# Kernel optimization log

Hardware: AMD Instinct MI355X
Metric: run time of the kernel (lower is better)

The kernel has to match this reference:

```python
import jax, jax.numpy as jnp
import numpy as np

N_NODES = 100000
N_EDGES = 1600000
IN_SIZE = 256
HID = 64
HEADS = 2
OUT_SIZE = 16


def _gat_layer(x, W, a_l, a_r, b, src, dst, n_nodes, heads, feat):
    # x: [N, Din]; W: [Din, H*F]; a_l, a_r: [H, F]; b: [H*F]
    h = (x @ W).reshape(n_nodes, heads, feat)          # [N, H, F]
    el = jnp.sum(h * a_l, axis=-1)                     # [N, H]
    er = jnp.sum(h * a_r, axis=-1)                     # [N, H]
    e = jax.nn.leaky_relu(el[src] + er[dst], 0.2)      # [E, H]
    # segment softmax over incoming edges of each dst node
    m = jax.ops.segment_max(e, dst, num_segments=n_nodes)
    m = jnp.where(jnp.isfinite(m), m, 0.0)             # nodes with no in-edges
    p = jnp.exp(e - m[dst])                            # [E, H]
    s = jax.ops.segment_sum(p, dst, num_segments=n_nodes)
    alpha = p / (s[dst] + 1e-9)                        # [E, H]
    # scatter-add weighted source features
    out = jax.ops.segment_sum(alpha[:, :, None] * h[src], dst, num_segments=n_nodes)
    return out + b.reshape(1, heads, feat)             # [N, H, F]


def setup_inputs() -> dict:
    key = jax.random.key(0)
    ks = jax.random.split(key, 12)
    features = jax.random.normal(ks[0], (N_NODES, IN_SIZE), dtype=jnp.float32)
    src = jax.random.randint(ks[1], (N_EDGES,), 0, N_NODES, dtype=jnp.int32)
    dst = jax.random.randint(ks[2], (N_EDGES,), 0, N_NODES, dtype=jnp.int32)
    s1 = 1.0 / np.sqrt(IN_SIZE)
    s2 = 1.0 / np.sqrt(HID * HEADS)
    W1 = jax.random.normal(ks[3], (IN_SIZE, HEADS * HID), dtype=jnp.float32) * s1
    al1 = jax.random.normal(ks[4], (HEADS, HID), dtype=jnp.float32) * 0.1
    ar1 = jax.random.normal(ks[5], (HEADS, HID), dtype=jnp.float32) * 0.1
    b1 = jnp.zeros((HEADS * HID,), dtype=jnp.float32)
    W2 = jax.random.normal(ks[6], (HEADS * HID, HEADS * HID), dtype=jnp.float32) * s2
    al2 = jax.random.normal(ks[7], (HEADS, HID), dtype=jnp.float32) * 0.1
    ar2 = jax.random.normal(ks[8], (HEADS, HID), dtype=jnp.float32) * 0.1
    b2 = jnp.zeros((HEADS * HID,), dtype=jnp.float32)
    Wl = jax.random.normal(ks[9], (HEADS * HID, OUT_SIZE), dtype=jnp.float32) * s2
    bl = jnp.zeros((OUT_SIZE,), dtype=jnp.float32)
    return {"features": features, "src": src, "dst": dst,
            "W1": W1, "al1": al1, "ar1": ar1, "b1": b1,
            "W2": W2, "al2": al2, "ar2": ar2, "b2": b2,
            "Wl": Wl, "bl": bl}


def reference(features, src, dst, W1, al1, ar1, b1, W2, al2, ar2, b2, Wl, bl):
    n = features.shape[0]
    h = _gat_layer(features, W1, al1, ar1, b1.reshape(HEADS, HID).reshape(-1),
                   src, dst, n, HEADS, HID)
    h = jax.nn.elu(h.reshape(n, HEADS * HID))          # flatten(1) + ELU (dropout: eval)
    h = _gat_layer(h, W2, al2, ar2, b2, src, dst, n, HEADS, HID)
    h = jax.nn.elu(h.reshape(n, HEADS * HID))
    return h @ Wl + bl                                  # [N, OUT_SIZE]
```

## Files before the change

### kernel.cpp

```cpp
#include <hip/hip_runtime.h>
#include <hip/hip_fp16.h>

#define N_NODES 100000
#define N_EDGES 1600000
#define IN_SIZE 256
#define HID 64
#define HEADS 2
#define DMODEL 128
#define OUT_SZ 16

#define BSHIFT 9
#define BNODES 512
#define NB 196
#define CAP 16384
#define EPB 4096

typedef _Float16 f16x4 __attribute__((ext_vector_type(4)));
typedef _Float16 f16x8 __attribute__((ext_vector_type(8)));
typedef float f32x4 __attribute__((ext_vector_type(4)));


__global__ __launch_bounds__(256) void wt_fused_kernel(const float* __restrict__ W1,
                                                       _Float16* __restrict__ Wt1,
                                                       const float* __restrict__ W2,
                                                       _Float16* __restrict__ Wt2,
                                                       int* __restrict__ counts) {
    int tid = threadIdx.x;
    if (blockIdx.x == 0 && tid < NB) counts[tid] = 0;
    int i = blockIdx.x * 256 + tid;
    if (i < 128 * IN_SIZE) {
        int nr = i / IN_SIZE;
        int k = i - nr * IN_SIZE;
        Wt1[i] = (_Float16)W1[(size_t)k * 128 + nr];
    } else {
        int j = i - 128 * IN_SIZE;
        if (j < 128 * DMODEL) {
            int nr = j / DMODEL;
            int k = j - nr * DMODEL;
            Wt2[j] = (_Float16)W2[(size_t)k * 128 + nr];
        }
    }
}


__global__ __launch_bounds__(256) void bin_kernel(const int* __restrict__ src,
                                                  const int* __restrict__ dst,
                                                  int* __restrict__ counts,
                                                  int2* __restrict__ bucketbuf, int e) {
    __shared__ int hist[NB];
    __shared__ int base[NB];
    int tid = threadIdx.x;
    int start = blockIdx.x * EPB;
    for (int i = tid; i < NB; i += 256) hist[i] = 0;
    __syncthreads();
    int pack[16];
    #pragma unroll
    for (int i = 0; i < 16; i++) {
        int idx = start + i * 256 + tid;
        int p = -1;
        if (idx < e) {
            int b = dst[idx] >> BSHIFT;
            int r = atomicAdd(&hist[b], 1);
            p = (b << 16) | r;
        }
        pack[i] = p;
    }
    __syncthreads();
    for (int i = tid; i < NB; i += 256)
        base[i] = atomicAdd(&counts[i], hist[i]);
    __syncthreads();
    #pragma unroll
    for (int i = 0; i < 16; i++) {
        int idx = start + i * 256 + tid;
        int p = pack[i];
        if (p >= 0) {
            int b = p >> 16;
            int pos = base[b] + (p & 0xffff);
            if (pos < CAP)
                bucketbuf[(size_t)b * CAP + pos] = make_int2(src[idx], dst[idx]);
        }
    }
}


__global__ __launch_bounds__(256) void csr_kernel(const int2* __restrict__ bucketbuf,
                                                  const int* __restrict__ counts,
                                                  int* __restrict__ deg,
                                                  int* __restrict__ offs,
                                                  int* __restrict__ ssrc, int n) {
    __shared__ int hist[BNODES];
    __shared__ int cursor[BNODES];
    __shared__ int lds[256];
    int b = blockIdx.x;
    int tid = threadIdx.x;

    int t = (tid < NB) ? min(counts[tid], CAP) : 0;
    lds[tid] = t;
    __syncthreads();
    for (int off = 1; off < 256; off <<= 1) {
        int x = 0;
        if (tid >= off) x = lds[tid - off];
        __syncthreads();
        lds[tid] += x;
        __syncthreads();
    }
    int base = (b == 0) ? 0 : lds[b - 1];
    int cnt = min(counts[b], CAP);
    __syncthreads();

    int node0 = b << BSHIFT;
    const int2* ebuf = bucketbuf + (size_t)b * CAP;

    hist[tid] = 0;
    hist[tid + 256] = 0;
    __syncthreads();
    for (int i = tid; i < cnt; i += 256)
        atomicAdd(&hist[ebuf[i].y - node0], 1);
    __syncthreads();

    int h0 = hist[2 * tid], h1 = hist[2 * tid + 1];
    lds[tid] = h0 + h1;
    __syncthreads();
    for (int off = 1; off < 256; off <<= 1) {
        int x = 0;
        if (tid >= off) x = lds[tid - off];
        __syncthreads();
        lds[tid] += x;
        __syncthreads();
    }
    int excl = lds[tid] - (h0 + h1);
    cursor[2 * tid] = excl;
    cursor[2 * tid + 1] = excl + h0;
    int g0 = node0 + 2 * tid, g1 = g0 + 1;
    if (g0 < n) { deg[g0] = h0; offs[g0] = base + excl; }
    if (g1 < n) { deg[g1] = h1; offs[g1] = base + excl + h0; }
    __syncthreads();

    for (int i = tid; i < cnt; i += 256) {
        int2 ed = ebuf[i];
        int p = atomicAdd(&cursor[ed.y - node0], 1);
        ssrc[base + p] = ed.x;
    }
}


template <int K, bool F16IN>
__global__ __launch_bounds__(256) void gemm_attn_kernel(const void* __restrict__ Ap,
                                                        const _Float16* __restrict__ Wt,
                                                        const float* __restrict__ al,
                                                        const float* __restrict__ ar,
                                                        uint32_t* __restrict__ h16,
                                                        float* __restrict__ el,
                                                        float* __restrict__ er, int n) {
    __shared__ _Float16 As[64 * 72];
    __shared__ _Float16 Bs[128 * 72];
    int tid = threadIdx.x;
    int w = tid >> 6;
    int lane = tid & 63;
    int c = lane & 15;
    int quad = lane >> 4;
    int r0 = blockIdx.x * 64;

    f32x4 acc[8];
    #pragma unroll
    for (int t = 0; t < 8; t++) acc[t] = (f32x4){0.f, 0.f, 0.f, 0.f};

    for (int kt = 0; kt < K; kt += 64) {
        {
            int lr = tid >> 4;
            int lc = (tid & 15) * 4;
            #pragma unroll
            for (int q = 0; q < 4; q++) {
                int row = lr + 16 * q;
                int gr = r0 + row;
                if constexpr (F16IN) {
                    const uint32_t* Af = (const uint32_t*)Ap;
                    uint2 v = make_uint2(0u, 0u);
                    if (gr < n) v = *(const uint2*)(Af + (size_t)gr * (K / 2) + (kt + lc) / 2);
                    *(uint2*)(As + row * 72 + lc) = v;
                } else {
                    const float* Af = (const float*)Ap;
                    float4 v = make_float4(0.f, 0.f, 0.f, 0.f);
                    if (gr < n) v = *(const float4*)(Af + (size_t)gr * K + kt + lc);
                    f16x4 hv = {(_Float16)v.x, (_Float16)v.y, (_Float16)v.z, (_Float16)v.w};
                    *(f16x4*)(As + row * 72 + lc) = hv;
                }
            }
            int nr = tid >> 1;
            int kc = (tid & 1) * 32;
            const uint4* gsrc = (const uint4*)(Wt + (size_t)nr * K + kt + kc);
            uint4 v0 = gsrc[0];
            uint4 v1 = gsrc[1];
            uint4 v2 = gsrc[2];
            uint4 v3 = gsrc[3];
            *(uint4*)(Bs + nr * 72 + kc + 0)  = v0;
            *(uint4*)(Bs + nr * 72 + kc + 8)  = v1;
            *(uint4*)(Bs + nr * 72 + kc + 16) = v2;
            *(uint4*)(Bs + nr * 72 + kc + 24) = v3;
        }
        __syncthreads();

        #pragma unroll
        for (int kk = 0; kk < 64; kk += 32) {
            f16x8 a = *(const f16x8*)(As + (16 * w + c) * 72 + kk + quad * 8);
            #pragma unroll
            for (int t = 0; t < 8; t++) {
                f16x8 b = *(const f16x8*)(Bs + (16 * t + c) * 72 + kk + quad * 8);
                acc[t] = __builtin_amdgcn_mfma_f32_16x16x32_f16(a, b, acc[t], 0, 0, 0);
            }
        }
        __syncthreads();
    }

    #pragma unroll
    for (int i = 0; i < 4; i++) {
        int gr = r0 + 16 * w + quad * 4 + i;
        float el0 = 0.f, el1 = 0.f, er0 = 0.f, er1 = 0.f;
        #pragma unroll
        for (int t = 0; t < 8; t++) {
            float hv = acc[t][i];
            float alv = al[16 * t + c];
            float arv = ar[16 * t + c];
            if (t < 4) { el0 += hv * alv; er0 += hv * arv; }
            else       { el1 += hv * alv; er1 += hv * arv; }
        }
        #pragma unroll
        for (int off = 1; off < 16; off <<= 1) {
            el0 += __shfl_xor(el0, off);
            el1 += __shfl_xor(el1, off);
            er0 += __shfl_xor(er0, off);
            er1 += __shfl_xor(er1, off);
        }
        if (c == 0 && gr < n) {
            *(float2*)(el + 2 * gr) = make_float2(el0, el1);
            *(float2*)(er + 2 * gr) = make_float2(er0, er1);
        }
        #pragma unroll
        for (int t = 0; t < 8; t++) {
            float own = acc[t][i];
            float other = __shfl_xor(own, 1);
            if ((c & 1) == 0 && gr < n) {
                __half2 hh = __floats2half2_rn(own, other);
                h16[(size_t)gr * 64 + 8 * t + (c >> 1)] = *(const uint32_t*)&hh;
            }
        }
    }
}


__device__ __forceinline__ float edge_w(float2 e, float erh, int head) {
    float x = (head ? e.y : e.x) + erh;
    x = x >= 0.f ? x : 0.2f * x;
    return __expf(x);
}

__device__ __forceinline__ void acc8(uint4 u, float w, float* a) {
    union { uint4 u4; f16x8 h8; } cv;
    cv.u4 = u;
    #pragma unroll
    for (int i = 0; i < 8; i++)
        a[i] = fmaf((float)cv.h8[i], w, a[i]);
}

__global__ __launch_bounds__(256) void agg_kernel(const uint32_t* __restrict__ hb,
                                                  const int* __restrict__ ssrc,
                                                  const float* __restrict__ el,
                                                  const float* __restrict__ er,
                                                  const float* __restrict__ bias,
                                                  const int* __restrict__ offs,
                                                  const int* __restrict__ deg,
                                                  uint32_t* __restrict__ out16, int n) {
    int wid = (blockIdx.x * blockDim.x + threadIdx.x) >> 6;
    int lane = threadIdx.x & 63;
    if (wid >= n) return;
    int start = offs[wid];
    int d = deg[wid];
    int g = lane >> 4;
    int fl = lane & 15;
    int head = fl >> 3;

    float2 erv = *(const float2*)(er + 2 * wid);
    float erh = head ? erv.y : erv.x;

    const int* sp = ssrc + start;
    const float2* el2 = (const float2*)el;
    const char* hbb = (const char*)hb;
    uint32_t foff = (uint32_t)(fl << 4);

    float a[8];
    #pragma unroll
    for (int i = 0; i < 8; i++) a[i] = 0.f;
    float psum = 0.f;

    int j = 0;
    if (d >= 16) {
        int s0 = sp[g];
        int s1 = sp[4 + g];
        int s2 = sp[8 + g];
        int s3 = sp[12 + g];
        for (; j + 32 <= d; j += 16) {
            float2 e0 = el2[s0];
            uint4 u0 = *(const uint4*)(hbb + (((uint32_t)s0 << 8) + foff));
            float2 e1 = el2[s1];
            uint4 u1 = *(const uint4*)(hbb + (((uint32_t)s1 << 8) + foff));
            float2 e2 = el2[s2];
            uint4 u2 = *(const uint4*)(hbb + (((uint32_t)s2 << 8) + foff));
            float2 e3 = el2[s3];
            uint4 u3 = *(const uint4*)(hbb + (((uint32_t)s3 << 8) + foff));
            int ns0 = sp[j + 16 + g];
            int ns1 = sp[j + 20 + g];
            int ns2 = sp[j + 24 + g];
            int ns3 = sp[j + 28 + g];
            float w0 = edge_w(e0, erh, head);
            float w1 = edge_w(e1, erh, head);
            float w2 = edge_w(e2, erh, head);
            float w3 = edge_w(e3, erh, head);
            psum += (w0 + w1) + (w2 + w3);
            acc8(u0, w0, a);
            acc8(u1, w1, a);
            acc8(u2, w2, a);
            acc8(u3, w3, a);
            s0 = ns0; s1 = ns1; s2 = ns2; s3 = ns3;
        }
        {
            float2 e0 = el2[s0];
            uint4 u0 = *(const uint4*)(hbb + (((uint32_t)s0 << 8) + foff));
            float2 e1 = el2[s1];
            uint4 u1 = *(const uint4*)(hbb + (((uint32_t)s1 << 8) + foff));
            float2 e2 = el2[s2];
            uint4 u2 = *(const uint4*)(hbb + (((uint32_t)s2 << 8) + foff));
            float2 e3 = el2[s3];
            uint4 u3 = *(const uint4*)(hbb + (((uint32_t)s3 << 8) + foff));
            float w0 = edge_w(e0, erh, head);
            float w1 = edge_w(e1, erh, head);
            float w2 = edge_w(e2, erh, head);
            float w3 = edge_w(e3, erh, head);
            psum += (w0 + w1) + (w2 + w3);
            acc8(u0, w0, a);
            acc8(u1, w1, a);
            acc8(u2, w2, a);
            acc8(u3, w3, a);
            j += 16;
        }
    }
    if (j < d) {
        int last = d - 1;
        int i0 = j + g, i1 = j + 4 + g, i2 = j + 8 + g, i3 = j + 12 + g;
        int s0 = sp[min(i0, last)];
        int s1 = sp[min(i1, last)];
        int s2 = sp[min(i2, last)];
        int s3 = sp[min(i3, last)];
        float2 e0 = el2[s0];
        uint4 u0 = *(const uint4*)(hbb + (((uint32_t)s0 << 8) + foff));
        float2 e1 = el2[s1];
        uint4 u1 = *(const uint4*)(hbb + (((uint32_t)s1 << 8) + foff));
        float2 e2 = el2[s2];
        uint4 u2 = *(const uint4*)(hbb + (((uint32_t)s2 << 8) + foff));
        float2 e3 = el2[s3];
        uint4 u3 = *(const uint4*)(hbb + (((uint32_t)s3 << 8) + foff));
        float w0 = (i0 <= last) ? edge_w(e0, erh, head) : 0.f;
        float w1 = (i1 <= last) ? edge_w(e1, erh, head) : 0.f;
        float w2 = (i2 <= last) ? edge_w(e2, erh, head) : 0.f;
        float w3 = (i3 <= last) ? edge_w(e3, erh, head) : 0.f;
        psum += (w0 + w1) + (w2 + w3);
        acc8(u0, w0, a);
        acc8(u1, w1, a);
        acc8(u2, w2, a);
        acc8(u3, w3, a);
    }

    #pragma unroll
    for (int i = 0; i < 8; i++) {
        a[i] += __shfl_xor(a[i], 16);
        a[i] += __shfl_xor(a[i], 32);
    }
    psum += __shfl_xor(psum, 16);
    psum += __shfl_xor(psum, 32);

    if (lane < 16) {
        float inv = 1.f / (psum + 1e-9f);
        float4 b0 = *(const float4*)(bias + 8 * lane);
        float4 b1 = *(const float4*)(bias + 8 * lane + 4);
        float o[8];
        o[0] = fmaf(a[0], inv, b0.x);
        o[1] = fmaf(a[1], inv, b0.y);
        o[2] = fmaf(a[2], inv, b0.z);
        o[3] = fmaf(a[3], inv, b0.w);
        o[4] = fmaf(a[4], inv, b1.x);
        o[5] = fmaf(a[5], inv, b1.y);
        o[6] = fmaf(a[6], inv, b1.z);
        o[7] = fmaf(a[7], inv, b1.w);
        #pragma unroll
        for (int i = 0; i < 8; i++)
            o[i] = o[i] > 0.f ? o[i] : (__expf(o[i]) - 1.f);
        __half2 h01 = __floats2half2_rn(o[0], o[1]);
        __half2 h23 = __floats2half2_rn(o[2], o[3]);
        __half2 h45 = __floats2half2_rn(o[4], o[5]);
        __half2 h67 = __floats2half2_rn(o[6], o[7]);
        uint4 ov = make_uint4(*(const uint32_t*)&h01, *(const uint32_t*)&h23,
                              *(const uint32_t*)&h45, *(const uint32_t*)&h67);
        ((uint4*)(out16 + (size_t)wid * 64))[lane] = ov;
    }
}


__global__ __launch_bounds__(256) void final_kernel(const uint32_t* __restrict__ x16,
                                                    const float* __restrict__ Wl,
                                                    const float* __restrict__ bl,
                                                    float* __restrict__ out, int n) {
    __shared__ float Ws[DMODEL * OUT_SZ];
    __shared__ float bs[OUT_SZ];
    int tid = threadIdx.x;
    for (int i = tid; i < DMODEL * OUT_SZ / 4; i += 256)
        ((float4*)Ws)[i] = ((const float4*)Wl)[i];
    if (tid < OUT_SZ) bs[tid] = bl[tid];
    __syncthreads();
    int node = blockIdx.x * 16 + (tid >> 4);
    int c = tid & 15;
    if (node >= n) return;
    const uint2* xr = (const uint2*)(x16 + (size_t)node * 64);
    float acc = bs[c];
    #pragma unroll
    for (int kk = 0; kk < 32; kk++) {
        uint2 v = xr[kk];
        float2 f0 = __half22float2(*(const __half2*)&v.x);
        float2 f1 = __half22float2(*(const __half2*)&v.y);
        acc += f0.x * Ws[(4 * kk + 0) * OUT_SZ + c];
        acc += f0.y * Ws[(4 * kk + 1) * OUT_SZ + c];
        acc += f1.x * Ws[(4 * kk + 2) * OUT_SZ + c];
        acc += f1.y * Ws[(4 * kk + 3) * OUT_SZ + c];
    }
    out[(size_t)node * OUT_SZ + c] = acc;
}


extern "C" void kernel_launch(void* const* d_in, const int* in_sizes, int n_in,
                              void* d_out, int out_size, void* d_ws, size_t ws_size,
                              hipStream_t stream) {
    const float* features = (const float*)d_in[0];
    const int*   src      = (const int*)d_in[1];
    const int*   dst      = (const int*)d_in[2];
    const float* W1  = (const float*)d_in[3];
    const float* al1 = (const float*)d_in[4];
    const float* ar1 = (const float*)d_in[5];
    const float* b1  = (const float*)d_in[6];
    const float* W2  = (const float*)d_in[7];
    const float* al2 = (const float*)d_in[8];
    const float* ar2 = (const float*)d_in[9];
    const float* b2  = (const float*)d_in[10];
    const float* Wl  = (const float*)d_in[11];
    const float* bl  = (const float*)d_in[12];
    float* out = (float*)d_out;

    const int n = N_NODES, e = N_EDGES;

    char* w = (char*)d_ws;
    uint32_t* h16 = (uint32_t*)w;       w += (size_t)n * 64 * 4;
    uint32_t* x1  = (uint32_t*)w;       w += (size_t)n * 64 * 4;
    uint32_t* x2  = (uint32_t*)w;       w += 26 * 1024 * 1024;
    float* el   = (float*)w;            w += (size_t)n * 2 * 4;
    float* er   = (float*)w;            w += (size_t)n * 2 * 4;
    int* deg    = (int*)w;              w += 400128;
    int* offs   = (int*)w;              w += 400128;
    int* ssrc   = (int*)w;              w += (size_t)e * 4;
    int* counts = (int*)w;              w += 1024;
    _Float16* Wt1 = (_Float16*)w;       w += 128 * IN_SIZE * 2;
    _Float16* Wt2 = (_Float16*)w;       w += 128 * DMODEL * 2;
    int2* bucketbuf = (int2*)x2;

    const int binBlocks = (e + EPB - 1) / EPB;
    const int wtBlocks = (128 * IN_SIZE + 128 * DMODEL + 255) / 256;
    const int gemmBlocks = (n + 63) / 64;
    const int aggBlocks = (n + 3) / 4;
    const int finalBlocks = (n + 15) / 16;

    wt_fused_kernel<<<wtBlocks, 256, 0, stream>>>(W1, Wt1, W2, Wt2, counts);

    bin_kernel<<<binBlocks, 256, 0, stream>>>(src, dst, counts, bucketbuf, e);
    csr_kernel<<<NB, 256, 0, stream>>>(bucketbuf, counts, deg, offs, ssrc, n);

    gemm_attn_kernel<IN_SIZE, false><<<gemmBlocks, 256, 0, stream>>>(features, Wt1, al1, ar1,
                                                                     h16, el, er, n);
    agg_kernel<<<aggBlocks, 256, 0, stream>>>(h16, ssrc, el, er, b1, offs, deg, x1, n);

    gemm_attn_kernel<DMODEL, true><<<gemmBlocks, 256, 0, stream>>>(x1, Wt2, al2, ar2,
                                                                   h16, el, er, n);
    agg_kernel<<<aggBlocks, 256, 0, stream>>>(h16, ssrc, el, er, b2, offs, deg, x2, n);

    final_kernel<<<finalBlocks, 256, 0, stream>>>(x2, Wl, bl, out, n);

    (void)in_sizes; (void)n_in; (void)out_size; (void)ws_size;
}
```

Before: 421.5 us.

## Pack bucketed edges into 32-bit words and stage scatter through LDS

```diff
diff --git a/kernel.cpp b/kernel.cpp
--- a/kernel.cpp
+++ b/kernel.cpp
@@ -18,6 +18,7 @@
 typedef _Float16 f16x4 __attribute__((ext_vector_type(4)));
 typedef _Float16 f16x8 __attribute__((ext_vector_type(8)));
 typedef float f32x4 __attribute__((ext_vector_type(4)));
+
 
 
 __global__ __launch_bounds__(256) void wt_fused_kernel(const float* __restrict__ W1,
@@ -46,44 +47,67 @@
 __global__ __launch_bounds__(256) void bin_kernel(const int* __restrict__ src,
                                                   const int* __restrict__ dst,
                                                   int* __restrict__ counts,
-                                                  int2* __restrict__ bucketbuf, int e) {
+                                                  uint32_t* __restrict__ bucketbuf, int e) {
     __shared__ int hist[NB];
-    __shared__ int base[NB];
+    __shared__ int lbase[NB + 1];
+    __shared__ int gbase[NB];
+    __shared__ uint32_t sbuf[EPB];
+    __shared__ int lds[256];
     int tid = threadIdx.x;
     int start = blockIdx.x * EPB;
     for (int i = tid; i < NB; i += 256) hist[i] = 0;
     __syncthreads();
-    int pack[16];
+    int pr[16];
+    uint32_t pv[16];
     #pragma unroll
     for (int i = 0; i < 16; i++) {
         int idx = start + i * 256 + tid;
-        int p = -1;
+        pr[i] = -1;
         if (idx < e) {
-            int b = dst[idx] >> BSHIFT;
+            int d = dst[idx];
+            int s = src[idx];
+            int b = d >> BSHIFT;
             int r = atomicAdd(&hist[b], 1);
-            p = (b << 16) | r;
-        }
-        pack[i] = p;
-    }
-    __syncthreads();
-    for (int i = tid; i < NB; i += 256)
-        base[i] = atomicAdd(&counts[i], hist[i]);
+            pr[i] = (b << 16) | r;
+            pv[i] = ((uint32_t)(d & (BNODES - 1)) << 17) | (uint32_t)s;
+        }
+    }
+    __syncthreads();
+    int h = (tid < NB) ? hist[tid] : 0;
+    lds[tid] = h;
+    __syncthreads();
+    for (int off = 1; off < 256; off <<= 1) {
+        int x = 0;
+        if (tid >= off) x = lds[tid - off];
+        __syncthreads();
+        lds[tid] += x;
+        __syncthreads();
+    }
+    if (tid < NB) lbase[tid] = lds[tid] - h;
+    if (tid == NB - 1) lbase[NB] = lds[tid];
+    if (tid < NB) gbase[tid] = atomicAdd(&counts[tid], h);
     __syncthreads();
     #pragma unroll
     for (int i = 0; i < 16; i++) {
-        int idx = start + i * 256 + tid;
-        int p = pack[i];
-        if (p >= 0) {
-            int b = p >> 16;
-            int pos = base[b] + (p & 0xffff);
-            if (pos < CAP)
-                bucketbuf[(size_t)b * CAP + pos] = make_int2(src[idx], dst[idx]);
-        }
-    }
-}
-
-
-__global__ __launch_bounds__(256) void csr_kernel(const int2* __restrict__ bucketbuf,
+        int p = pr[i];
+        if (p >= 0) sbuf[lbase[p >> 16] + (p & 0xffff)] = pv[i];
+    }
+    __syncthreads();
+    int total = lbase[NB];
+    for (int i = tid; i < total; i += 256) {
+        int lo = 0, hi = NB - 1;
+        while (lo < hi) {
+            int mid = (lo + hi + 1) >> 1;
+            if (lbase[mid] <= i) lo = mid; else hi = mid - 1;
+        }
+        int posg = gbase[lo] + (i - lbase[lo]);
+        if (posg < CAP)
+            bucketbuf[(size_t)lo * CAP + posg] = sbuf[i];
+    }
+}
+
+
+__global__ __launch_bounds__(256) void csr_kernel(const uint32_t* __restrict__ bucketbuf,
                                                   const int* __restrict__ counts,
                                                   int* __restrict__ deg,
                                                   int* __restrict__ offs,
@@ -109,13 +133,13 @@
     __syncthreads();
 
     int node0 = b << BSHIFT;
-    const int2* ebuf = bucketbuf + (size_t)b * CAP;
+    const uint32_t* ebuf = bucketbuf + (size_t)b * CAP;
 
     hist[tid] = 0;
     hist[tid + 256] = 0;
     __syncthreads();
     for (int i = tid; i < cnt; i += 256)
-        atomicAdd(&hist[ebuf[i].y - node0], 1);
+        atomicAdd(&hist[ebuf[i] >> 17], 1);
     __syncthreads();
 
     int h0 = hist[2 * tid], h1 = hist[2 * tid + 1];
@@ -137,9 +161,9 @@
     __syncthreads();
 
     for (int i = tid; i < cnt; i += 256) {
-        int2 ed = ebuf[i];
-        int p = atomicAdd(&cursor[ed.y - node0], 1);
-        ssrc[base + p] = ed.x;
+        uint32_t ed = ebuf[i];
+        int p = atomicAdd(&cursor[ed >> 17], 1);
+        ssrc[base + p] = (int)(ed & 0x1FFFF);
     }
 }
 
@@ -343,30 +367,15 @@
             j += 16;
         }
     }
-    if (j < d) {
+    for (; j < d; j += 4) {
         int last = d - 1;
-        int i0 = j + g, i1 = j + 4 + g, i2 = j + 8 + g, i3 = j + 12 + g;
+        int i0 = j + g;
         int s0 = sp[min(i0, last)];
-        int s1 = sp[min(i1, last)];
-        int s2 = sp[min(i2, last)];
-        int s3 = sp[min(i3, last)];
         float2 e0 = el2[s0];
         uint4 u0 = *(const uint4*)(hbb + (((uint32_t)s0 << 8) + foff));
-        float2 e1 = el2[s1];
-        uint4 u1 = *(const uint4*)(hbb + (((uint32_t)s1 << 8) + foff));
-        float2 e2 = el2[s2];
-        uint4 u2 = *(const uint4*)(hbb + (((uint32_t)s2 << 8) + foff));
-        float2 e3 = el2[s3];
-        uint4 u3 = *(const uint4*)(hbb + (((uint32_t)s3 << 8) + foff));
         float w0 = (i0 <= last) ? edge_w(e0, erh, head) : 0.f;
-        float w1 = (i1 <= last) ? edge_w(e1, erh, head) : 0.f;
-        float w2 = (i2 <= last) ? edge_w(e2, erh, head) : 0.f;
-        float w3 = (i3 <= last) ? edge_w(e3, erh, head) : 0.f;
-        psum += (w0 + w1) + (w2 + w3);
+        psum += w0;
         acc8(u0, w0, a);
-        acc8(u1, w1, a);
-        acc8(u2, w2, a);
-        acc8(u3, w3, a);
     }
 
     #pragma unroll
@@ -418,17 +427,23 @@
     int node = blockIdx.x * 16 + (tid >> 4);
     int c = tid & 15;
     if (node >= n) return;
-    const uint2* xr = (const uint2*)(x16 + (size_t)node * 64);
+    const uint4* xr = (const uint4*)(x16 + (size_t)node * 64);
     float acc = bs[c];
     #pragma unroll
-    for (int kk = 0; kk < 32; kk++) {
-        uint2 v = xr[kk];
+    for (int kk = 0; kk < 16; kk++) {
+        uint4 v = xr[kk];
         float2 f0 = __half22float2(*(const __half2*)&v.x);
         float2 f1 = __half22float2(*(const __half2*)&v.y);
-        acc += f0.x * Ws[(4 * kk + 0) * OUT_SZ + c];
-        acc += f0.y * Ws[(4 * kk + 1) * OUT_SZ + c];
-        acc += f1.x * Ws[(4 * kk + 2) * OUT_SZ + c];
-        acc += f1.y * Ws[(4 * kk + 3) * OUT_SZ + c];
+        float2 f2 = __half22float2(*(const __half2*)&v.z);
+        float2 f3 = __half22float2(*(const __half2*)&v.w);
+        acc += f0.x * Ws[(8 * kk + 0) * OUT_SZ + c];
+        acc += f0.y * Ws[(8 * kk + 1) * OUT_SZ + c];
+        acc += f1.x * Ws[(8 * kk + 2) * OUT_SZ + c];
+        acc += f1.y * Ws[(8 * kk + 3) * OUT_SZ + c];
+        acc += f2.x * Ws[(8 * kk + 4) * OUT_SZ + c];
+        acc += f2.y * Ws[(8 * kk + 5) * OUT_SZ + c];
+        acc += f3.x * Ws[(8 * kk + 6) * OUT_SZ + c];
+        acc += f3.y * Ws[(8 * kk + 7) * OUT_SZ + c];
     }
     out[(size_t)node * OUT_SZ + c] = acc;
 }
@@ -466,7 +481,7 @@
     int* counts = (int*)w;              w += 1024;
     _Float16* Wt1 = (_Float16*)w;       w += 128 * IN_SIZE * 2;
     _Float16* Wt2 = (_Float16*)w;       w += 128 * DMODEL * 2;
-    int2* bucketbuf = (int2*)x2;
+    uint32_t* bucketbuf = (uint32_t*)x2;
 
     const int binBlocks = (e + EPB - 1) / EPB;
     const int wtBlocks = (128 * IN_SIZE + 128 * DMODEL + 255) / 256;
```

New measurement: 427.3 us. Within noise of the previous version (+1.4%).
